# Optimization experiments

Hardware: AMD Instinct MI355X
Metric: run time of the kernel (lower is better)

## Reference

```python
import jax, jax.numpy as jnp
import numpy as np

# irreps = 128x0e + 64x1e + 32x2e
NUM_SCALAR = 128
VEC_MULS = [(64, 3), (32, 5)]  # (multiplicity, ir.dim)
NUM_VECTOR = sum(m for m, _ in VEC_MULS)          # 96
NUM_FEATURES = NUM_SCALAR + NUM_VECTOR            # 224
TOTAL_DIM = NUM_SCALAR + sum(m * d for m, d in VEC_MULS)  # 480
GATE_IN = NUM_SCALAR + NUM_VECTOR                 # 224
BN_DIM = int(GATE_IN * 0.5)                       # 112
EPS = 1e-6
N = 200000


def _build_indices():
    scalar_idx, scalar_ch, vector_idx, vector_ch_local, ch_expand = [], [], [], [], []
    ch, vec_ch, offset = 0, 0, 0
    for _ in range(NUM_SCALAR):
        scalar_idx.append(offset); scalar_ch.append(ch); ch_expand.append(ch)
        offset += 1; ch += 1
    for mul, dim in VEC_MULS:
        for _ in range(mul):
            for _ in range(dim):
                vector_idx.append(offset); vector_ch_local.append(vec_ch); ch_expand.append(ch)
                offset += 1
            vec_ch += 1; ch += 1
    f = lambda a: jnp.asarray(np.array(a, dtype=np.int32))
    return f(scalar_idx), f(scalar_ch), f(vector_idx), f(vector_ch_local), f(ch_expand)


def setup_inputs() -> dict:
    key = jax.random.key(0)
    ks = jax.random.split(key, 8)
    scalar_idx, scalar_ch, vector_idx, vector_ch_local, ch_expand = _build_indices()
    s = lambda fan_in: 1.0 / np.sqrt(fan_in)
    return {
        "x": jax.random.normal(ks[0], (N, TOTAL_DIM), dtype=jnp.float32),
        "W1": jax.random.normal(ks[1], (GATE_IN, BN_DIM), dtype=jnp.float32) * s(GATE_IN),
        "b1": jax.random.normal(ks[2], (BN_DIM,), dtype=jnp.float32) * 0.01,
        "W2": jax.random.normal(ks[3], (BN_DIM, NUM_FEATURES), dtype=jnp.float32) * s(BN_DIM),
        "b2": jax.random.normal(ks[4], (NUM_FEATURES,), dtype=jnp.float32) * 0.01,
        "affine_weight": jnp.ones((1, NUM_FEATURES), dtype=jnp.float32)
                         + 0.02 * jax.random.normal(ks[5], (1, NUM_FEATURES), dtype=jnp.float32),
        "affine_bias": 0.02 * jax.random.normal(ks[6], (1, NUM_SCALAR), dtype=jnp.float32),
        "scalar_idx": scalar_idx,
        "scalar_ch": scalar_ch,
        "vector_idx": vector_idx,
        "vector_ch_local": vector_ch_local,
        "ch_expand": ch_expand,
    }


def reference(x, W1, b1, W2, b2, affine_weight, affine_bias,
              scalar_idx, scalar_ch, vector_idx, vector_ch_local, ch_expand):
    # ---- scalar channels: center across scalar channels per row
    scalars = x[:, scalar_idx]                                   # [N, S]
    scalars_centered = scalars - scalars.mean(axis=1, keepdims=True)
    # ---- vector channels: per-vector-channel RMS via segment mean over components
    vec_sq = x[:, vector_idx] ** 2                               # [N, Vtot]
    seg_sum = jax.ops.segment_sum(vec_sq.T, vector_ch_local, num_segments=NUM_VECTOR).T  # [N, V]
    counts = jax.ops.segment_sum(jnp.ones_like(vector_ch_local, dtype=x.dtype),
                                 vector_ch_local, num_segments=NUM_VECTOR)               # [V]
    vectors_rms = jnp.sqrt(seg_sum / counts + EPS)               # [N, V]
    # ---- gated bottleneck MLP (gate_norm == 'none')
    gate_in = jnp.concatenate([scalars_centered, vectors_rms], axis=1)  # [N, S+V]
    h = jax.nn.silu(gate_in @ W1 + b1)
    gate_scores = 2.0 * jax.nn.sigmoid(h @ W2 + b2)              # [N, F]
    gate_scores = gate_scores * affine_weight
    # ---- scatter gated affine back to the full irreps layout
    x_out = x * gate_scores[:, ch_expand]                        # [N, D]
    scalar_out = scalars_centered * gate_scores[:, scalar_ch] + affine_bias
    x_out = x_out.at[:, scalar_idx].set(scalar_out)
    return x_out
```

## Files before the change

kernel.cpp:

```cpp
#include <hip/hip_runtime.h>
#include <math.h>

#define NS 128
#define TD 480
#define NF 224
#define BN 112
#define TM 64
#define K1 224
#define K1S 232
#define K2S 136
#define GS 225
#define W1T_ELEMS (BN * K1S)
#define W2T_ELEMS (NF * K2S)

typedef __bf16 bf16x8 __attribute__((ext_vector_type(8)));
typedef float f32x4 __attribute__((ext_vector_type(4)));

__device__ __forceinline__ unsigned short f2bf(float f) {
  union { float f; unsigned u; } v; v.f = f;
  unsigned r = v.u + 0x7FFFu + ((v.u >> 16) & 1u);
  return (unsigned short)(r >> 16);
}

struct SMemA {
  unsigned short gateA[TM * K1S];
  unsigned short hA[TM * K2S];
  float rowbuf[4][352];
};
struct __align__(16) SMem {
  union {
    SMemA a;
    float gates[TM * GS];
  };
  float absb[NS];
  float meanv[TM];
};

__global__ void prep_kernel(const float* __restrict__ W1, const float* __restrict__ W2,
                            unsigned short* __restrict__ w1t, unsigned short* __restrict__ w2t) {
  int t = blockIdx.x * 256 + threadIdx.x;
  if (t < W1T_ELEMS) {
    int n = t / K1S, k = t - n * K1S;
    float v = (k < K1) ? W1[k * BN + n] : 0.0f;
    w1t[t] = f2bf(v);
  } else {
    int t2 = t - W1T_ELEMS;
    if (t2 < W2T_ELEMS) {
      int n = t2 / K2S, k = t2 - n * K2S;
      float v = (k < BN) ? W2[k * NF + n] : 0.0f;
      w2t[t2] = f2bf(v);
    }
  }
}

__global__ __launch_bounds__(256, 2) void fused_kernel(
    const float* __restrict__ X,
    const float* __restrict__ b1, const float* __restrict__ b2,
    const float* __restrict__ aw, const float* __restrict__ ab,
    const unsigned short* __restrict__ w1t, const unsigned short* __restrict__ w2t,
    float* __restrict__ OUT) {
  __shared__ SMem sm;
  const int tid  = threadIdx.x;
  const int lane = tid & 63;
  const int w    = tid >> 6;
  const int l15  = lane & 15;
  const int quad = lane >> 4;
  const int R0   = blockIdx.x * TM;

  if (lane < 32) sm.absb[32 * w + lane] = ab[32 * w + lane];

  if (lane < 32) {
    int r = 16 * w + (lane >> 1);
    *(f32x4*)&sm.a.hA[r * K2S + 112 + 8 * (lane & 1)] = (f32x4){0.f, 0.f, 0.f, 0.f};
  }

  {
    f32x4 cur0, cur1, nxt0, nxt1;
    const int rbase = 16 * w;
    auto loadRow = [&](int rl, f32x4& a0, f32x4& a1) {
      const float* rp = X + (size_t)(R0 + rl) * TD;
      a0 = *(const f32x4*)(rp + 4 * lane);
      if (lane < 56) a1 = *(const f32x4*)(rp + 256 + 4 * lane);
    };
    auto procRow = [&](int rl, f32x4 v0, f32x4 v1) {
      float ssum = (lane < 32) ? (v0[0] + v0[1] + v0[2] + v0[3]) : 0.0f;
      #pragma unroll
      for (int m = 32; m >= 1; m >>= 1) ssum += __shfl_xor(ssum, m, 64);
      float mean = ssum * (1.0f / 128.0f);
      float* rb = sm.a.rowbuf[w];
      if (lane >= 32) {
        f32x4 sq;
        #pragma unroll
        for (int j = 0; j < 4; ++j) sq[j] = v0[j] * v0[j];
        *(f32x4*)&rb[4 * (lane - 32)] = sq;
      }
      if (lane < 56) {
        f32x4 sq;
        #pragma unroll
        for (int j = 0; j < 4; ++j) sq[j] = v1[j] * v1[j];
        *(f32x4*)&rb[128 + 4 * lane] = sq;
      }
      __builtin_amdgcn_wave_barrier();
      float s3 = rb[3 * lane] + rb[3 * lane + 1] + rb[3 * lane + 2];
      float r3 = sqrtf(s3 * (1.0f / 3.0f) + 1e-6f);
      unsigned short* ga = &sm.a.gateA[rl * K1S];
      if (lane < 32) {
        ushort4 pk;
        pk.x = f2bf(v0[0] - mean); pk.y = f2bf(v0[1] - mean);
        pk.z = f2bf(v0[2] - mean); pk.w = f2bf(v0[3] - mean);
        *(ushort4*)&ga[4 * lane] = pk;
      }
      ga[128 + lane] = f2bf(r3);
      if (lane < 32) {
        float s5 = 0.0f;
        #pragma unroll
        for (int q = 0; q < 5; ++q) s5 += rb[192 + 5 * lane + q];
        ga[192 + lane] = f2bf(sqrtf(s5 * 0.2f + 1e-6f));
      }
      if (lane == 0) sm.meanv[rl] = mean;
      __builtin_amdgcn_wave_barrier();
    };
    loadRow(rbase, cur0, cur1);
    #pragma unroll
    for (int i = 0; i < 16; ++i) {
      if (i < 15) loadRow(rbase + i + 1, nxt0, nxt1);
      procRow(rbase + i, cur0, cur1);
      cur0 = nxt0; cur1 = nxt1;
    }
  }

  {
    f32x4 acc[7];
    #pragma unroll
    for (int j = 0; j < 7; ++j) acc[j] = (f32x4){0.f, 0.f, 0.f, 0.f};
    const unsigned short* gA = &sm.a.gateA[(16 * w + l15) * K1S];
    const unsigned short* B1p = w1t + l15 * K1S + quad * 8;
    #pragma unroll
    for (int kk = 0; kk < 7; ++kk) {
      bf16x8 a = *(const bf16x8*)(gA + kk * 32 + quad * 8);
      #pragma unroll
      for (int nb = 0; nb < 7; ++nb) {
        bf16x8 bb = *(const bf16x8*)(B1p + nb * 16 * K1S + kk * 32);
        acc[nb] = __builtin_amdgcn_mfma_f32_16x16x32_bf16(a, bb, acc[nb], 0, 0, 0);
      }
    }
    #pragma unroll
    for (int nb = 0; nb < 7; ++nb) {
      int n = nb * 16 + l15;
      float bias = b1[n];
      #pragma unroll
      for (int i = 0; i < 4; ++i) {
        int r = 16 * w + quad * 4 + i;
        float hv = acc[nb][i] + bias;
        float sg = 1.0f / (1.0f + __expf(-hv));
        sm.a.hA[r * K2S + n] = f2bf(hv * sg);
      }
    }
  }

  float garr[56];
  {
    f32x4 acc[14];
    #pragma unroll
    for (int j = 0; j < 14; ++j) acc[j] = (f32x4){0.f, 0.f, 0.f, 0.f};
    const unsigned short* hAp = &sm.a.hA[(16 * w + l15) * K2S];
    const unsigned short* B2p = w2t + l15 * K2S + quad * 8;
    #pragma unroll
    for (int kk = 0; kk < 4; ++kk) {
      bf16x8 a = *(const bf16x8*)(hAp + kk * 32 + quad * 8);
      #pragma unroll
      for (int nb = 0; nb < 14; ++nb) {
        bf16x8 bb = *(const bf16x8*)(B2p + nb * 16 * K2S + kk * 32);
        acc[nb] = __builtin_amdgcn_mfma_f32_16x16x32_bf16(a, bb, acc[nb], 0, 0, 0);
      }
    }
    #pragma unroll
    for (int nb = 0; nb < 14; ++nb) {
      int n = nb * 16 + l15;
      float b2v = b2[n], awv = aw[n];
      #pragma unroll
      for (int i = 0; i < 4; ++i) {
        float z = acc[nb][i] + b2v;
        garr[nb * 4 + i] = 2.0f * awv / (1.0f + __expf(-z));
      }
    }
  }

  __syncthreads();
  #pragma unroll
  for (int nb = 0; nb < 14; ++nb) {
    #pragma unroll
    for (int i = 0; i < 4; ++i) {
      int r = 16 * w + quad * 4 + i;
      sm.gates[r * GS + nb * 16 + l15] = garr[nb * 4 + i];
    }
  }
  __syncthreads();

  const float* Xb = X + (size_t)R0 * TD;
  float* Ob = OUT + (size_t)R0 * TD;
  #pragma unroll 5
  for (int it = 0; it < 30; ++it) {
    int u = tid + it * 256;
    int e = u * 4;
    int r = e / TD;
    int c = e - r * TD;
    f32x4 xv = *(const f32x4*)(Xb + e);
    float m = sm.meanv[r];
    float out[4];
    #pragma unroll
    for (int i = 0; i < 4; ++i) {
      int ci = c + i;
      int ch = (ci < NS) ? ci
             : ((ci < 320) ? (NS + (ci - NS) / 3) : (192 + (ci - 320) / 5));
      float g = sm.gates[r * GS + ch];
      out[i] = (ci < NS) ? ((xv[i] - m) * g + sm.absb[ci]) : (xv[i] * g);
    }
    f32x4 ov = {out[0], out[1], out[2], out[3]};
    __builtin_nontemporal_store(ov, (f32x4*)(Ob + e));
  }
}

extern "C" void kernel_launch(void* const* d_in, const int* in_sizes, int n_in,
                              void* d_out, int out_size, void* d_ws, size_t ws_size,
                              hipStream_t stream) {
  const float* X  = (const float*)d_in[0];
  const float* W1 = (const float*)d_in[1];
  const float* b1 = (const float*)d_in[2];
  const float* W2 = (const float*)d_in[3];
  const float* b2 = (const float*)d_in[4];
  const float* aw = (const float*)d_in[5];
  const float* ab = (const float*)d_in[6];
  float* OUT = (float*)d_out;
  unsigned short* w1t = (unsigned short*)d_ws;
  unsigned short* w2t = w1t + W1T_ELEMS;

  int n = in_sizes[0] / TD;
  int pb = (W1T_ELEMS + W2T_ELEMS + 255) / 256;
  hipLaunchKernelGGL(prep_kernel, dim3(pb), dim3(256), 0, stream, W1, W2, w1t, w2t);
  hipLaunchKernelGGL(fused_kernel, dim3(n / TM), dim3(256), 0, stream,
                     X, b1, b2, aw, ab, w1t, w2t, OUT);
}
```

Before: 811.3 us.

## Halve gate staging buffer, raise occupancy, and prefetch X before barriers

Shrinks the shared gate buffer to hold 32 rows and writes the gates in two halves, so LDS per block falls and launch bounds can target three blocks per CU. The row-statistics loop now prefetches two rows ahead, and X tiles for each half are loaded with nontemporal loads before the barriers, so memory latency overlaps the gate writes. In exchange it adds two extra block barriers and more live registers, which may be hard to fit under the tighter register budget and could cause spills.

Result: faster. 765.1 us (-5.7%).

```diff
diff --git a/kernel.cpp b/kernel.cpp
--- a/kernel.cpp
+++ b/kernel.cpp
@@ -30,7 +30,7 @@
 struct __align__(16) SMem {
   union {
     SMemA a;
-    float gates[TM * GS];
+    float gates[32 * GS];
   };
   float absb[NS];
   float meanv[TM];
@@ -53,7 +53,7 @@
   }
 }
 
-__global__ __launch_bounds__(256, 2) void fused_kernel(
+__global__ __launch_bounds__(256, 3) void fused_kernel(
     const float* __restrict__ X,
     const float* __restrict__ b1, const float* __restrict__ b2,
     const float* __restrict__ aw, const float* __restrict__ ab,
@@ -75,12 +75,12 @@
   }
 
   {
-    f32x4 cur0, cur1, nxt0, nxt1;
+    f32x4 a0, a1, bb0, bb1, c0, c1;
     const int rbase = 16 * w;
-    auto loadRow = [&](int rl, f32x4& a0, f32x4& a1) {
+    auto loadRow = [&](int rl, f32x4& v0, f32x4& v1) {
       const float* rp = X + (size_t)(R0 + rl) * TD;
-      a0 = *(const f32x4*)(rp + 4 * lane);
-      if (lane < 56) a1 = *(const f32x4*)(rp + 256 + 4 * lane);
+      v0 = *(const f32x4*)(rp + 4 * lane);
+      if (lane < 56) v1 = *(const f32x4*)(rp + 256 + 4 * lane);
     };
     auto procRow = [&](int rl, f32x4 v0, f32x4 v1) {
       float ssum = (lane < 32) ? (v0[0] + v0[1] + v0[2] + v0[3]) : 0.0f;
@@ -120,12 +120,13 @@
       if (lane == 0) sm.meanv[rl] = mean;
       __builtin_amdgcn_wave_barrier();
     };
-    loadRow(rbase, cur0, cur1);
+    loadRow(rbase, a0, a1);
+    loadRow(rbase + 1, bb0, bb1);
     #pragma unroll
     for (int i = 0; i < 16; ++i) {
-      if (i < 15) loadRow(rbase + i + 1, nxt0, nxt1);
-      procRow(rbase + i, cur0, cur1);
-      cur0 = nxt0; cur1 = nxt1;
+      if (i < 14) loadRow(rbase + i + 2, c0, c1);
+      procRow(rbase + i, a0, a1);
+      a0 = bb0; a1 = bb1; bb0 = c0; bb1 = c1;
     }
   }
 
@@ -186,39 +187,64 @@
     }
   }
 
-  __syncthreads();
-  #pragma unroll
-  for (int nb = 0; nb < 14; ++nb) {
-    #pragma unroll
-    for (int i = 0; i < 4; ++i) {
-      int r = 16 * w + quad * 4 + i;
-      sm.gates[r * GS + nb * 16 + l15] = garr[nb * 4 + i];
-    }
-  }
-  __syncthreads();
-
   const float* Xb = X + (size_t)R0 * TD;
   float* Ob = OUT + (size_t)R0 * TD;
-  #pragma unroll 5
-  for (int it = 0; it < 30; ++it) {
-    int u = tid + it * 256;
-    int e = u * 4;
-    int r = e / TD;
-    int c = e - r * TD;
-    f32x4 xv = *(const f32x4*)(Xb + e);
-    float m = sm.meanv[r];
-    float out[4];
-    #pragma unroll
-    for (int i = 0; i < 4; ++i) {
-      int ci = c + i;
-      int ch = (ci < NS) ? ci
-             : ((ci < 320) ? (NS + (ci - NS) / 3) : (192 + (ci - 320) / 5));
-      float g = sm.gates[r * GS + ch];
-      out[i] = (ci < NS) ? ((xv[i] - m) * g + sm.absb[ci]) : (xv[i] * g);
-    }
-    f32x4 ov = {out[0], out[1], out[2], out[3]};
-    __builtin_nontemporal_store(ov, (f32x4*)(Ob + e));
-  }
+
+  auto writeGates = [&]() {
+    int rl = 16 * (w & 1) + quad * 4;
+    #pragma unroll
+    for (int nb = 0; nb < 14; ++nb) {
+      #pragma unroll
+      for (int i = 0; i < 4; ++i)
+        sm.gates[(rl + i) * GS + nb * 16 + l15] = garr[nb * 4 + i];
+    }
+  };
+
+  f32x4 pre[5];
+  auto preload = [&](const float* Xh) {
+    #pragma unroll
+    for (int it = 0; it < 5; ++it)
+      pre[it] = __builtin_nontemporal_load((const f32x4*)(Xh + 4 * (tid + it * 256)));
+  };
+  auto doHalf = [&](int h, const float* Xh, float* Oh) {
+    const int roff = h * 32;
+    auto proc = [&](f32x4 xv, int u) {
+      int e = u * 4;
+      int r = e / TD;
+      int c = e - r * TD;
+      float m = sm.meanv[r + roff];
+      float out[4];
+      #pragma unroll
+      for (int i = 0; i < 4; ++i) {
+        int ci = c + i;
+        int ch = (ci < NS) ? ci
+               : ((ci < 320) ? (NS + (ci - NS) / 3) : (192 + (ci - 320) / 5));
+        float g = sm.gates[r * GS + ch];
+        out[i] = (ci < NS) ? ((xv[i] - m) * g + sm.absb[ci]) : (xv[i] * g);
+      }
+      f32x4 ov = {out[0], out[1], out[2], out[3]};
+      __builtin_nontemporal_store(ov, (f32x4*)(Oh + e));
+    };
+    #pragma unroll
+    for (int it = 0; it < 5; ++it) proc(pre[it], tid + it * 256);
+    #pragma unroll 5
+    for (int it = 5; it < 15; ++it) {
+      int u = tid + it * 256;
+      f32x4 xv = __builtin_nontemporal_load((const f32x4*)(Xh + 4 * u));
+      proc(xv, u);
+    }
+  };
+
+  preload(Xb);
+  __syncthreads();
+  if ((w >> 1) == 0) writeGates();
+  __syncthreads();
+  doHalf(0, Xb, Ob);
+  preload(Xb + 32 * TD);
+  __syncthreads();
+  if ((w >> 1) == 1) writeGates();
+  __syncthreads();
+  doHalf(1, Xb + 32 * TD, Ob + 32 * TD);
 }
 
 extern "C" void kernel_launch(void* const* d_in, const int* in_sizes, int n_in,
```
